# Performance work log

Measured on AMD Instinct MI355X. Metric: run time of the kernel, lower is better.

## Reference

```python
import jax, jax.numpy as jnp
import numpy as np

N = 16384      # points
F = 16         # input feature dim
ATT = 32       # attention_dim == d_model of positional encoding
NFREQ = 64     # num_freq_bands
MAXFREQ = 10.0
K = 32         # knn k
B = 8          # number of graphs in batch
FEAT_DIM = F + ATT   # 48
POS_DIM = 3 + ATT    # 35


def setup_inputs() -> dict:
    key = jax.random.key(0)
    ks = jax.random.split(key, 12)
    x = jax.random.normal(ks[0], (N, F), dtype=jnp.float32)
    pos = jax.random.normal(ks[1], (N, 3), dtype=jnp.float32) * 3.0
    batch = jnp.sort(jax.random.randint(ks[2], (N,), 0, B)).astype(jnp.int64)
    def lin(k1, k2, fin, fout):
        w = jax.random.normal(k1, (fin, fout), dtype=jnp.float32) / np.sqrt(fin)
        b = jax.random.normal(k2, (fout,), dtype=jnp.float32) * 0.01
        return w, b
    w1f, b1f = lin(ks[3], ks[4], FEAT_DIM, ATT)
    w2f, b2f = lin(ks[5], ks[6], ATT, 1)
    w1p, b1p = lin(ks[7], ks[8], POS_DIM, ATT)
    w2p, b2p = lin(ks[9], ks[10], ATT, 1)
    return {"x": x, "pos": pos, "batch": batch,
            "w1f": w1f, "b1f": b1f, "w2f": w2f, "b2f": b2f,
            "w1p": w1p, "b1p": b1p, "w2p": w2p, "b2p": b2p}


def _positional_encoding(xyz):
    # [N,3] -> [N, ATT]; sin/cos interleaved over linspace freq bands, truncated
    fb = jnp.linspace(1.0, MAXFREQ, NFREQ).astype(xyz.dtype)       # [NFREQ]
    xf = xyz[:, :, None] * fb                                      # [N,3,NFREQ]
    enc = jnp.stack([jnp.sin(xf), jnp.cos(xf)], axis=-1)           # [N,3,NFREQ,2]
    enc = enc.reshape(xyz.shape[0], -1)                            # [N, 3*NFREQ*2]
    return enc[:, :ATT]


def _combined_normalized(x, pos, batch, w1f, b1f, w2f, b2f, w1p, b1p, w2p, b2p):
    xyz = pos[:, :3]
    enc = _positional_encoding(xyz)
    feat = jnp.concatenate([x, enc], axis=-1)      # [N, FEAT_DIM]
    pe = jnp.concatenate([xyz, enc], axis=-1)      # [N, POS_DIM]
    # AdaptiveBlending: two tiny MLPs -> softmax over 2 logits
    fw = jnp.maximum(feat @ w1f + b1f, 0.0) @ w2f + b2f   # [N,1]
    pw = jnp.maximum(pe @ w1p + b1p, 0.0) @ w2p + b2p     # [N,1]
    sw = jax.nn.softmax(jnp.concatenate([fw, pw], axis=-1), axis=-1)  # [N,2]
    combined = jnp.concatenate([pe * sw[:, 1:2], feat * sw[:, 0:1]], axis=-1)  # [N, POS+FEAT]
    # batch_normalize: per-graph scatter mean / unbiased std (torch_scatter default)
    ones = jnp.ones((combined.shape[0],), combined.dtype)
    cnt = jax.ops.segment_sum(ones, batch, num_segments=B)[:, None]     # [B,1]
    s = jax.ops.segment_sum(combined, batch, num_segments=B)            # [B,D]
    mean = s / jnp.maximum(cnt, 1.0)
    ss = jax.ops.segment_sum(combined * combined, batch, num_segments=B)
    var = (ss - cnt * mean * mean) / jnp.maximum(cnt - 1.0, 1.0)
    std = jnp.sqrt(jnp.clip(var, 0.0))
    return (combined - mean[batch]) / (std[batch] + 1e-8)


def reference(x, pos, batch, w1f, b1f, w2f, b2f, w1p, b1p, w2p, b2p):
    z = _combined_normalized(x, pos, batch, w1f, b1f, w2f, b2f, w1p, b1p, w2p, b2p)
    # focal_points = all points; per-batch masked KNN over squared distances
    sq = jnp.sum(z * z, axis=-1)                                    # [N]
    d2 = sq[:, None] + sq[None, :] - 2.0 * (z @ z.T)                # [N,N]
    same = batch[:, None] == batch[None, :]
    d2 = jnp.where(same, d2, jnp.inf)
    _, idx = jax.lax.top_k(-d2, K)                                  # [N,K]
    row = jnp.repeat(jnp.arange(z.shape[0], dtype=jnp.int64), K)    # query index
    col = idx.reshape(-1).astype(jnp.int64)                         # neighbor index
    return row, col
```

## Files before the change

### kernel.cpp

```cpp
#include <hip/hip_runtime.h>
#include <math.h>

#define NPTS 16384
#define KNN 32
#define NB 8
#define CD 83
#define CDP 84
#define PDIM 35
#define QPB 16
#define NSL 8
#define MST 33

__device__ __forceinline__ int bval(const int* __restrict__ p, int i, int is32) {
    return is32 ? p[i] : p[2 * i];
}

__device__ __forceinline__ float np_sincos_f32(float x, int compute_cos) {
    const float two_over_pi = 0x1.45f306p-1f;
    const float c1 = -0x1.921fb0p+00f;
    const float c2 = -0x1.5110b4p-22f;
    const float c3 = -0x1.846988p-48f;
    const float rint_cvt = 12582912.0f;
    float q = __fsub_rn(__fadd_rn(__fmul_rn(x, two_over_pi), rint_cvt), rint_cvt);
    float rx = __builtin_fmaf(q, c1, x);
    rx = __builtin_fmaf(q, c2, rx);
    rx = __builtin_fmaf(q, c3, rx);
    float r2 = __fmul_rn(rx, rx);
    float yc = __builtin_fmaf(0x1.98e616p-16f, r2, -0x1.6c06dcp-10f);
    yc = __builtin_fmaf(yc, r2, 0x1.55553cp-05f);
    yc = __builtin_fmaf(yc, r2, -0x1.000000p-1f);
    yc = __builtin_fmaf(yc, r2, 0x1.000000p+0f);
    float ys = __builtin_fmaf(0x1.7d3bbcp-19f, r2, -0x1.a06bbap-13f);
    ys = __builtin_fmaf(ys, r2, 0x1.11119ap-07f);
    ys = __builtin_fmaf(ys, r2, -0x1.555556p-03f);
    ys = __fmul_rn(ys, r2);
    ys = __builtin_fmaf(ys, rx, rx);
    int iq = (int)q + compute_cos;
    float res = ((iq & 1) == 0) ? ys : yc;
    if (iq & 2) res = __int_as_float(__float_as_int(res) ^ 0x80000000u);
    return res;
}

__device__ __forceinline__ float np_exp_f32(float x) {
    const float log2e = 1.442695040f;
    const float rint_cvt = 12582912.0f;
    if (x < -87.33654f) return 0.0f;
    float q = __fsub_rn(__fadd_rn(__fmul_rn(x, log2e), rint_cvt), rint_cvt);
    float r = __builtin_fmaf(q, -0.693359375f, x);
    r = __builtin_fmaf(q, 2.12194440e-4f, r);
    float y = 1.9875691500e-4f;
    y = __builtin_fmaf(y, r, 1.3981999507e-3f);
    y = __builtin_fmaf(y, r, 8.3334519073e-3f);
    y = __builtin_fmaf(y, r, 4.1665795894e-2f);
    y = __builtin_fmaf(y, r, 1.6666665459e-1f);
    y = __builtin_fmaf(y, r, 5.0000001201e-1f);
    float r2 = __fmul_rn(r, r);
    y = __builtin_fmaf(y, r2, r);
    y = __fadd_rn(y, 1.0f);
    int iq = (int)q;
    float sc = __int_as_float((127 + iq) << 23);
    return __fmul_rn(y, sc);
}

__device__ __forceinline__ float np_gemv32(const float* h, const float* __restrict__ w) {
    float a0 = 0.f, a1 = 0.f, a2 = 0.f, a3 = 0.f, a4 = 0.f, a5 = 0.f, a6 = 0.f, a7 = 0.f;
    #pragma unroll
    for (int t = 0; t < 32; t += 8) {
        a0 = __builtin_fmaf(h[t],     w[t],     a0);
        a1 = __builtin_fmaf(h[t + 1], w[t + 1], a1);
        a2 = __builtin_fmaf(h[t + 2], w[t + 2], a2);
        a3 = __builtin_fmaf(h[t + 3], w[t + 3], a3);
        a4 = __builtin_fmaf(h[t + 4], w[t + 4], a4);
        a5 = __builtin_fmaf(h[t + 5], w[t + 5], a5);
        a6 = __builtin_fmaf(h[t + 6], w[t + 6], a6);
        a7 = __builtin_fmaf(h[t + 7], w[t + 7], a7);
    }
    float s0 = __fadd_rn(a0, a4);
    float s1 = __fadd_rn(a1, a5);
    float s2 = __fadd_rn(a2, a6);
    float s3 = __fadd_rn(a3, a7);
    return __fadd_rn(__fadd_rn(s0, s1), __fadd_rn(s2, s3));
}

__global__ void k_flag(const int* __restrict__ batch32, int* __restrict__ flag) {
    if (threadIdx.x == 0) flag[0] = (batch32[NPTS - 1] != 0) ? 1 : 0;
}

__global__ void k_bounds(const int* __restrict__ batch, const int* __restrict__ flag,
                         int* __restrict__ seg) {
    int b = threadIdx.x;
    if (b > NB) return;
    int is32 = flag[0];
    int lo = 0, hi = NPTS;
    while (lo < hi) { int mid = (lo + hi) >> 1; if (bval(batch, mid, is32) < b) lo = mid + 1; else hi = mid; }
    seg[b] = lo;
}

__global__ void __launch_bounds__(256) k_front(
    const float* __restrict__ x, const float* __restrict__ pos,
    const float* __restrict__ w1f, const float* __restrict__ b1f,
    const float* __restrict__ w2f, const float* __restrict__ b2f,
    const float* __restrict__ w1p, const float* __restrict__ b1p,
    const float* __restrict__ w2p, const float* __restrict__ b2p,
    float* __restrict__ comb)
{
    __shared__ float s_w1f[48 * 32];
    __shared__ float s_w1p[35 * 32];
    __shared__ float s_b1f[32], s_w2f[32], s_b1p[32], s_w2p[32];
    __shared__ float s_b2[2];
    int t = threadIdx.x;
    for (int idx = t; idx < 48 * 32; idx += 256) s_w1f[idx] = w1f[idx];
    for (int idx = t; idx < 35 * 32; idx += 256) s_w1p[idx] = w1p[idx];
    if (t < 32) { s_b1f[t] = b1f[t]; s_w2f[t] = w2f[t]; s_b1p[t] = b1p[t]; s_w2p[t] = w2p[t]; }
    if (t == 0) { s_b2[0] = b2f[0]; s_b2[1] = b2p[0]; }
    __syncthreads();

    int i = blockIdx.x * 256 + t;

    float xr[16];
    const float4* x4 = (const float4*)(x + (long)i * 16);
    #pragma unroll
    for (int d4 = 0; d4 < 4; ++d4) {
        float4 v = x4[d4];
        xr[4 * d4] = v.x; xr[4 * d4 + 1] = v.y; xr[4 * d4 + 2] = v.z; xr[4 * d4 + 3] = v.w;
    }
    float p0 = pos[i * 3], p1 = pos[i * 3 + 1], p2 = pos[i * 3 + 2];

    float enc[32];
    #pragma unroll
    for (int f = 0; f < 16; ++f) {
        float fbf = (float)((double)f * (9.0 / 63.0) + 1.0);
        float a = __fmul_rn(p0, fbf);
        enc[2 * f] = np_sincos_f32(a, 0);
        enc[2 * f + 1] = np_sincos_f32(a, 1);
    }

    float h[32], hr[32];
    #pragma unroll
    for (int j = 0; j < 32; ++j) h[j] = 0.0f;
    #pragma unroll
    for (int k = 0; k < 16; ++k) {
        float v = xr[k];
        #pragma unroll
        for (int j = 0; j < 32; ++j) h[j] = __builtin_fmaf(v, s_w1f[k * 32 + j], h[j]);
    }
    for (int e = 0; e < 32; ++e) {
        float v = enc[e];
        #pragma unroll
        for (int j = 0; j < 32; ++j) h[j] = __builtin_fmaf(v, s_w1f[(16 + e) * 32 + j], h[j]);
    }
    #pragma unroll
    for (int j = 0; j < 32; ++j) hr[j] = fmaxf(__fadd_rn(h[j], s_b1f[j]), 0.0f);
    float fw = __fadd_rn(np_gemv32(hr, s_w2f), s_b2[0]);

    #pragma unroll
    for (int j = 0; j < 32; ++j) h[j] = 0.0f;
    {
        #pragma unroll
        for (int j = 0; j < 32; ++j) h[j] = __builtin_fmaf(p0, s_w1p[0 * 32 + j], h[j]);
        #pragma unroll
        for (int j = 0; j < 32; ++j) h[j] = __builtin_fmaf(p1, s_w1p[1 * 32 + j], h[j]);
        #pragma unroll
        for (int j = 0; j < 32; ++j) h[j] = __builtin_fmaf(p2, s_w1p[2 * 32 + j], h[j]);
    }
    for (int e = 0; e < 32; ++e) {
        float v = enc[e];
        #pragma unroll
        for (int j = 0; j < 32; ++j) h[j] = __builtin_fmaf(v, s_w1p[(3 + e) * 32 + j], h[j]);
    }
    #pragma unroll
    for (int j = 0; j < 32; ++j) hr[j] = fmaxf(__fadd_rn(h[j], s_b1p[j]), 0.0f);
    float pw = __fadd_rn(np_gemv32(hr, s_w2p), s_b2[1]);

    float m = fmaxf(fw, pw);
    float e0 = np_exp_f32(__fsub_rn(fw, m));
    float e1 = np_exp_f32(__fsub_rn(pw, m));
    float s = __fadd_rn(e0, e1);
    float sw0 = __fdiv_rn(e0, s);
    float sw1 = __fdiv_rn(e1, s);

    float* out = comb + (long)i * CDP;
    out[0] = __fmul_rn(p0, sw1);
    out[1] = __fmul_rn(p1, sw1);
    out[2] = __fmul_rn(p2, sw1);
    #pragma unroll
    for (int e = 0; e < 32; ++e) out[3 + e] = __fmul_rn(enc[e], sw1);
    #pragma unroll
    for (int k = 0; k < 16; ++k) out[35 + k] = __fmul_rn(xr[k], sw0);
    #pragma unroll
    for (int e = 0; e < 32; ++e) out[51 + e] = __fmul_rn(enc[e], sw0);
    out[83] = 0.0f;
}

__global__ void __launch_bounds__(128) k_stats(
    const float* __restrict__ comb, const int* __restrict__ seg,
    float* __restrict__ meanb, float* __restrict__ denb)
{
    int b = blockIdx.x;
    int d = threadIdx.x;
    if (d >= CD) return;
    int start = seg[b], end = seg[b + 1];
    float sum = 0.0f, ss = 0.0f;
    int r = start;
    for (; r + 8 <= end; r += 8) {
        float v0 = comb[(long)(r + 0) * CDP + d];
        float v1 = comb[(long)(r + 1) * CDP + d];
        float v2 = comb[(long)(r + 2) * CDP + d];
        float v3 = comb[(long)(r + 3) * CDP + d];
        float v4 = comb[(long)(r + 4) * CDP + d];
        float v5 = comb[(long)(r + 5) * CDP + d];
        float v6 = comb[(long)(r + 6) * CDP + d];
        float v7 = comb[(long)(r + 7) * CDP + d];
        sum = __fadd_rn(sum, v0); ss = __fadd_rn(ss, __fmul_rn(v0, v0));
        sum = __fadd_rn(sum, v1); ss = __fadd_rn(ss, __fmul_rn(v1, v1));
        sum = __fadd_rn(sum, v2); ss = __fadd_rn(ss, __fmul_rn(v2, v2));
        sum = __fadd_rn(sum, v3); ss = __fadd_rn(ss, __fmul_rn(v3, v3));
        sum = __fadd_rn(sum, v4); ss = __fadd_rn(ss, __fmul_rn(v4, v4));
        sum = __fadd_rn(sum, v5); ss = __fadd_rn(ss, __fmul_rn(v5, v5));
        sum = __fadd_rn(sum, v6); ss = __fadd_rn(ss, __fmul_rn(v6, v6));
        sum = __fadd_rn(sum, v7); ss = __fadd_rn(ss, __fmul_rn(v7, v7));
    }
    for (; r < end; ++r) {
        float c = comb[(long)r * CDP + d];
        sum = __fadd_rn(sum, c);
        ss = __fadd_rn(ss, __fmul_rn(c, c));
    }
    float cnt = (float)(end - start);
    float mn = __fdiv_rn(sum, fmaxf(cnt, 1.0f));
    float num = __fsub_rn(ss, __fmul_rn(__fmul_rn(cnt, mn), mn));
    float var = __fdiv_rn(num, fmaxf(__fsub_rn(cnt, 1.0f), 1.0f));
    if (var < 0.0f) var = 0.0f;
    meanb[b * CD + d] = mn;
    denb[b * CD + d] = __fadd_rn(__fsqrt_rn(var), 1e-8f);
}

__global__ void __launch_bounds__(256) k_z(
    float* __restrict__ comb, const int* __restrict__ batch, const int* __restrict__ flag,
    const float* __restrict__ meanb, const float* __restrict__ denb,
    float* __restrict__ sqb)
{
    int r = blockIdx.x * 256 + threadIdx.x;
    int b = bval(batch, r, flag[0]);
    const float* mb = meanb + b * CD;
    const float* db = denb + b * CD;
    float4* row4 = (float4*)(comb + (long)r * CDP);
    float rv[CDP];
    #pragma unroll
    for (int d4 = 0; d4 < 21; ++d4) {
        float4 v = row4[d4];
        rv[4 * d4] = v.x; rv[4 * d4 + 1] = v.y; rv[4 * d4 + 2] = v.z; rv[4 * d4 + 3] = v.w;
    }
    float p[CD];
    for (int d = 0; d < CD; ++d) {
        float zz = __fdiv_rn(__fsub_rn(rv[d], mb[d]), db[d]);
        rv[d] = zz;
        p[d] = __fmul_rn(zz, zz);
    }
    rv[83] = 0.0f;
    #pragma unroll
    for (int d4 = 0; d4 < 21; ++d4) {
        float4 v;
        v.x = rv[4 * d4]; v.y = rv[4 * d4 + 1]; v.z = rv[4 * d4 + 2]; v.w = rv[4 * d4 + 3];
        row4[d4] = v;
    }
    float r0 = p[0], r1 = p[1], r2 = p[2], r3 = p[3];
    float r4 = p[4], r5 = p[5], r6 = p[6], r7 = p[7];
    #pragma unroll
    for (int i = 8; i < 80; i += 8) {
        r0 = __fadd_rn(r0, p[i]);     r1 = __fadd_rn(r1, p[i + 1]);
        r2 = __fadd_rn(r2, p[i + 2]); r3 = __fadd_rn(r3, p[i + 3]);
        r4 = __fadd_rn(r4, p[i + 4]); r5 = __fadd_rn(r5, p[i + 5]);
        r6 = __fadd_rn(r6, p[i + 6]); r7 = __fadd_rn(r7, p[i + 7]);
    }
    float res = __fadd_rn(__fadd_rn(__fadd_rn(r0, r1), __fadd_rn(r2, r3)),
                          __fadd_rn(__fadd_rn(r4, r5), __fadd_rn(r6, r7)));
    res = __fadd_rn(res, p[80]);
    res = __fadd_rn(res, p[81]);
    res = __fadd_rn(res, p[82]);
    sqb[r] = res;
}

__global__ void __launch_bounds__(128) k_knn(
    const float* __restrict__ z, const float* __restrict__ sqb,
    const int* __restrict__ batch, const int* __restrict__ flag,
    const int* __restrict__ seg, int* __restrict__ out)
{
    __shared__ float s_kd[128 * MST];
    __shared__ int   s_ki[128 * MST];

    int t = threadIdx.x;
    int q = t >> 3, s = t & 7;
    int i = blockIdx.x * QPB + q;
    int is32 = flag[0];
    int bi = bval(batch, i, is32);
    int lo = seg[bi], hi = seg[bi + 1];

    float zq[CDP];
    const float4* z4 = (const float4*)(z + (long)i * CDP);
    #pragma unroll
    for (int d4 = 0; d4 < 21; ++d4) {
        float4 v = z4[d4];
        zq[4 * d4] = v.x; zq[4 * d4 + 1] = v.y; zq[4 * d4 + 2] = v.z; zq[4 * d4 + 3] = v.w;
    }
    float sqi = sqb[i];

    float kd[KNN]; int ki[KNN];
    #pragma unroll
    for (int k = 0; k < KNN; ++k) { kd[k] = INFINITY; ki[k] = 0x7fffffff; }

    for (int j = lo + s; j < hi; j += NSL) {
        const float4* zj4 = (const float4*)(z + (long)j * CDP);
        float acc = 0.0f;
        #pragma unroll
        for (int d4 = 0; d4 < 21; ++d4) {
            float4 v = zj4[d4];
            acc = __builtin_fmaf(zq[4 * d4],     v.x, acc);
            acc = __builtin_fmaf(zq[4 * d4 + 1], v.y, acc);
            acc = __builtin_fmaf(zq[4 * d4 + 2], v.z, acc);
            acc = __builtin_fmaf(zq[4 * d4 + 3], v.w, acc);
        }
        float dist = __fsub_rn(__fadd_rn(sqi, sqb[j]), __fmul_rn(2.0f, acc));
        if (dist < kd[KNN - 1] || (dist == kd[KNN - 1] && j < ki[KNN - 1])) {
            kd[KNN - 1] = dist; ki[KNN - 1] = j;
            #pragma unroll
            for (int k = KNN - 2; k >= 0; --k) {
                bool sw = (kd[k + 1] < kd[k]) || (kd[k + 1] == kd[k] && ki[k + 1] < ki[k]);
                if (sw) {
                    float td = kd[k]; kd[k] = kd[k + 1]; kd[k + 1] = td;
                    int ti = ki[k]; ki[k] = ki[k + 1]; ki[k + 1] = ti;
                }
            }
        }
    }

    #pragma unroll
    for (int k = 0; k < KNN; ++k) { s_kd[t * MST + k] = kd[k]; s_ki[t * MST + k] = ki[k]; }
    __syncthreads();

    if (s == 0) {
        int p[NSL];
        #pragma unroll
        for (int l = 0; l < NSL; ++l) p[l] = 0;
        int* orow = out;
        int* ocol = out + (long)NPTS * KNN;
        for (int k = 0; k < KNN; ++k) {
            float bd = INFINITY; int bix = 0x7fffffff; int bl = 0;
            #pragma unroll
            for (int l = 0; l < NSL; ++l) {
                int pp = p[l];
                float d = (pp < KNN) ? s_kd[(t + l) * MST + pp] : INFINITY;
                int  ii = (pp < KNN) ? s_ki[(t + l) * MST + pp] : 0x7fffffff;
                if (d < bd || (d == bd && ii < bix)) { bd = d; bix = ii; bl = l; }
            }
            #pragma unroll
            for (int l = 0; l < NSL; ++l) if (bl == l) p[l]++;
            orow[(long)i * KNN + k] = i;
            ocol[(long)i * KNN + k] = bix;
        }
    }
}

extern "C" void kernel_launch(void* const* d_in, const int* in_sizes, int n_in,
                              void* d_out, int out_size, void* d_ws, size_t ws_size,
                              hipStream_t stream)
{
    const float* x   = (const float*)d_in[0];
    const float* pos = (const float*)d_in[1];
    const int* batch = (const int*)d_in[2];
    const float* w1f = (const float*)d_in[3];
    const float* b1f = (const float*)d_in[4];
    const float* w2f = (const float*)d_in[5];
    const float* b2f = (const float*)d_in[6];
    const float* w1p = (const float*)d_in[7];
    const float* b1p = (const float*)d_in[8];
    const float* w2p = (const float*)d_in[9];
    const float* b2p = (const float*)d_in[10];

    char* ws = (char*)d_ws;
    float* comb  = (float*)(ws);
    float* sqb   = (float*)(ws + 5505024);
    float* meanb = (float*)(ws + 5570560);
    float* denb  = (float*)(ws + 5573216);
    int*   seg   = (int*)  (ws + 5575936);
    int*   flag  = (int*)  (ws + 5576000);
    int* out = (int*)d_out;

    hipLaunchKernelGGL(k_flag, dim3(1), dim3(64), 0, stream, batch, flag);
    hipLaunchKernelGGL(k_bounds, dim3(1), dim3(16), 0, stream, batch, flag, seg);
    hipLaunchKernelGGL(k_front, dim3(NPTS / 256), dim3(256), 0, stream,
                       x, pos, w1f, b1f, w2f, b2f, w1p, b1p, w2p, b2p, comb);
    hipLaunchKernelGGL(k_stats, dim3(NB), dim3(128), 0, stream, comb, seg, meanb, denb);
    hipLaunchKernelGGL(k_z, dim3(NPTS / 256), dim3(256), 0, stream, comb, batch, flag, meanb, denb, sqb);
    hipLaunchKernelGGL(k_knn, dim3(NPTS / QPB), dim3(128), 0, stream, comb, sqb, batch, flag, seg, out);
}
```

Baseline: 884.7 us.

## Pack distance and index into 64-bit sort keys and widen per-query slicing

Replaces the separate float-distance and int-index top-K lists with one sortable 64-bit key per entry, so each insertion step is a single unsigned compare and swap instead of a compound tie-break. Each query now gets 16 scanning lanes instead of 8, with 8 queries per block, which halves the candidate count per thread. The merge stage uses a smaller shared buffer split into two halves with extra barriers. The 64-bit keys double the register cost of each list, and the 16-way merge on a single thread per query does more serial work.

```diff
diff --git a/kernel.cpp b/kernel.cpp
--- a/kernel.cpp
+++ b/kernel.cpp
@@ -7,12 +7,20 @@
 #define CD 83
 #define CDP 84
 #define PDIM 35
-#define QPB 16
-#define NSL 8
+#define QPB 8
+#define NSL 16
 #define MST 33
+
+typedef unsigned long long ull;
 
 __device__ __forceinline__ int bval(const int* __restrict__ p, int i, int is32) {
     return is32 ? p[i] : p[2 * i];
+}
+
+__device__ __forceinline__ ull distkey(float d, int idx) {
+    unsigned u = __float_as_uint(d);
+    u = (u & 0x80000000u) ? ~u : (u | 0x80000000u);
+    return ((ull)u << 32) | (unsigned)idx;
 }
 
 __device__ __forceinline__ float np_sincos_f32(float x, int compute_cos) {
@@ -285,11 +293,10 @@
     const int* __restrict__ batch, const int* __restrict__ flag,
     const int* __restrict__ seg, int* __restrict__ out)
 {
-    __shared__ float s_kd[128 * MST];
-    __shared__ int   s_ki[128 * MST];
+    __shared__ ull s_kl[64 * MST];
 
     int t = threadIdx.x;
-    int q = t >> 3, s = t & 7;
+    int q = t >> 4, s = t & 15;
     int i = blockIdx.x * QPB + q;
     int is32 = flag[0];
     int bi = bval(batch, i, is32);
@@ -304,12 +311,13 @@
     }
     float sqi = sqb[i];
 
-    float kd[KNN]; int ki[KNN];
-    #pragma unroll
-    for (int k = 0; k < KNN; ++k) { kd[k] = INFINITY; ki[k] = 0x7fffffff; }
+    ull kl[KNN];
+    #pragma unroll
+    for (int k = 0; k < KNN; ++k) kl[k] = ~0ull;
 
     for (int j = lo + s; j < hi; j += NSL) {
         const float4* zj4 = (const float4*)(z + (long)j * CDP);
+        float sqj = sqb[j];
         float acc = 0.0f;
         #pragma unroll
         for (int d4 = 0; d4 < 21; ++d4) {
@@ -319,43 +327,46 @@
             acc = __builtin_fmaf(zq[4 * d4 + 2], v.z, acc);
             acc = __builtin_fmaf(zq[4 * d4 + 3], v.w, acc);
         }
-        float dist = __fsub_rn(__fadd_rn(sqi, sqb[j]), __fmul_rn(2.0f, acc));
-        if (dist < kd[KNN - 1] || (dist == kd[KNN - 1] && j < ki[KNN - 1])) {
-            kd[KNN - 1] = dist; ki[KNN - 1] = j;
+        float dist = __fsub_rn(__fadd_rn(sqi, sqj), __fmul_rn(2.0f, acc));
+        ull key = distkey(dist, j);
+        if (key < kl[KNN - 1]) {
+            kl[KNN - 1] = key;
             #pragma unroll
             for (int k = KNN - 2; k >= 0; --k) {
-                bool sw = (kd[k + 1] < kd[k]) || (kd[k + 1] == kd[k] && ki[k + 1] < ki[k]);
-                if (sw) {
-                    float td = kd[k]; kd[k] = kd[k + 1]; kd[k + 1] = td;
-                    int ti = ki[k]; ki[k] = ki[k + 1]; ki[k + 1] = ti;
-                }
+                if (kl[k + 1] < kl[k]) { ull tmp = kl[k]; kl[k] = kl[k + 1]; kl[k + 1] = tmp; }
             }
         }
     }
 
-    #pragma unroll
-    for (int k = 0; k < KNN; ++k) { s_kd[t * MST + k] = kd[k]; s_ki[t * MST + k] = ki[k]; }
-    __syncthreads();
-
-    if (s == 0) {
-        int p[NSL];
-        #pragma unroll
-        for (int l = 0; l < NSL; ++l) p[l] = 0;
-        int* orow = out;
-        int* ocol = out + (long)NPTS * KNN;
-        for (int k = 0; k < KNN; ++k) {
-            float bd = INFINITY; int bix = 0x7fffffff; int bl = 0;
+    int* orow = out;
+    int* ocol = out + (long)NPTS * KNN;
+    #pragma unroll
+    for (int half = 0; half < 2; ++half) {
+        __syncthreads();
+        if ((t >> 6) == half) {
+            int qh = q & 3;
             #pragma unroll
-            for (int l = 0; l < NSL; ++l) {
-                int pp = p[l];
-                float d = (pp < KNN) ? s_kd[(t + l) * MST + pp] : INFINITY;
-                int  ii = (pp < KNN) ? s_ki[(t + l) * MST + pp] : 0x7fffffff;
-                if (d < bd || (d == bd && ii < bix)) { bd = d; bix = ii; bl = l; }
+            for (int k = 0; k < KNN; ++k) s_kl[(s * 4 + qh) * MST + k] = kl[k];
+        }
+        __syncthreads();
+        if ((t >> 6) == half && s == 0) {
+            int qh = q & 3;
+            int p[NSL];
+            #pragma unroll
+            for (int l = 0; l < NSL; ++l) p[l] = 0;
+            for (int k = 0; k < KNN; ++k) {
+                ull best = ~0ull; int bl = 0;
+                #pragma unroll
+                for (int l = 0; l < NSL; ++l) {
+                    int pp = p[l];
+                    ull v = (pp < KNN) ? s_kl[(l * 4 + qh) * MST + pp] : ~0ull;
+                    if (v < best) { best = v; bl = l; }
+                }
+                #pragma unroll
+                for (int l = 0; l < NSL; ++l) if (bl == l) p[l]++;
+                orow[(long)i * KNN + k] = i;
+                ocol[(long)i * KNN + k] = (int)(best & 0xffffffffull);
             }
-            #pragma unroll
-            for (int l = 0; l < NSL; ++l) if (bl == l) p[l]++;
-            orow[(long)i * KNN + k] = i;
-            ocol[(long)i * KNN + k] = bix;
         }
     }
 }
```

Result: slower. 932.2 us (+5.4%).
